# Optimization experiments

Hardware: AMD Instinct MI355X
Metric: run time of the kernel (lower is better)

Reference implementation:

```python
import jax, jax.numpy as jnp
import numpy as np

B, S, D = 4, 4096, 2048
SCAN, STATE = 128, 16


def setup_inputs() -> dict:
    key = jax.random.key(0)
    ks = jax.random.split(key, 8)
    scale = 1.0 / np.sqrt(D)
    scale_s = 1.0 / np.sqrt(SCAN)
    x = jax.random.normal(ks[0], (B, S, D), dtype=jnp.float32)
    Wi = jax.random.normal(ks[1], (SCAN, D), dtype=jnp.float32) * scale
    Wo = jax.random.normal(ks[2], (D, SCAN), dtype=jnp.float32) * 0.02  # torch zero-inits; small random for nontrivial output
    A_log = jax.random.normal(ks[3], (SCAN, STATE), dtype=jnp.float32) * 0.1
    Wb = jax.random.normal(ks[4], (STATE, SCAN), dtype=jnp.float32) * scale_s
    Wc = jax.random.normal(ks[5], (STATE, SCAN), dtype=jnp.float32) * scale_s
    Wdt = jax.random.normal(ks[6], (SCAN, SCAN), dtype=jnp.float32) * scale_s
    b_dt = jnp.full((SCAN,), -3.0, dtype=jnp.float32)
    Wg = jax.random.normal(ks[7], (SCAN, D), dtype=jnp.float32) * scale
    return {"x": x, "Wi": Wi, "Wo": Wo, "A_log": A_log, "Wb": Wb,
            "Wc": Wc, "Wdt": Wdt, "b_dt": b_dt, "Wg": Wg}


def _selective_scan_ffn(x, Wi, Wo, A_log, Wb, Wc, Wdt, b_dt, Wg):
    z = jnp.einsum('bsd,nd->bsn', x, Wi)                      # [B,S,SCAN]
    gate = jax.nn.silu(jnp.einsum('bsd,nd->bsn', x, Wg))      # [B,S,SCAN]
    A = -jnp.exp(A_log)                                        # [SCAN,STATE]
    B_in = jnp.einsum('bsn,kn->bsk', z, Wb)                   # [B,S,STATE]
    C_in = jnp.einsum('bsn,kn->bsk', z, Wc)                   # [B,S,STATE]
    dt = jax.nn.softplus(jnp.einsum('bsn,mn->bsm', z, Wdt) + b_dt)  # [B,S,SCAN]
    A_bar = 1.0 + dt[..., None] * A                            # [B,S,SCAN,STATE]

    def step(state, inp):
        a_t, dt_t, z_t, b_t, c_t = inp
        # state: [B,SCAN,STATE]
        state = a_t * state + dt_t[..., None] * (z_t[..., None] * b_t[:, None, :])
        y = jnp.einsum('bnk,bk->bn', state, c_t)               # [B,SCAN]
        return state, y

    xs = (jnp.moveaxis(A_bar, 1, 0), jnp.moveaxis(dt, 1, 0),
          jnp.moveaxis(z, 1, 0), jnp.moveaxis(B_in, 1, 0), jnp.moveaxis(C_in, 1, 0))
    state0 = jnp.zeros((x.shape[0], Wi.shape[0], A_log.shape[1]), dtype=x.dtype)
    _, ys = jax.lax.scan(step, state0, xs)                     # [S,B,SCAN]
    y = jnp.moveaxis(ys, 0, 1) * gate                          # [B,S,SCAN]
    return jnp.einsum('bsn,dn->bsd', y, Wo)                    # [B,S,D]


def reference(x, Wi, Wo, A_log, Wb, Wc, Wdt, b_dt, Wg):
    return _selective_scan_ffn(x, Wi, Wo, A_log, Wb, Wc, Wdt, b_dt, Wg)
```

## Files before the change

### kernel.cpp

```cpp
#include <hip/hip_runtime.h>
#include <hip/hip_bf16.h>
#include <math.h>

using bf16 = __hip_bfloat16;
typedef __attribute__((ext_vector_type(8))) short bf16x8;
typedef __attribute__((ext_vector_type(8))) short short8;
typedef __attribute__((ext_vector_type(4))) short short4v;
typedef __attribute__((ext_vector_type(4))) float f32x4;

#define AS1 __attribute__((address_space(1)))
#define AS3 __attribute__((address_space(3)))

constexpr int BATCH = 4;
constexpr int SEQ   = 4096;
constexpr int DIM   = 2048;
constexpr int SCAN  = 128;
constexpr int STATE = 16;
constexpr int LCH   = 16;
constexpr int NCH   = SEQ / LCH;

__device__ __forceinline__ float bf2f(bf16 v) { return __bfloat162float(v); }
__device__ __forceinline__ bf16  f2bf(float v) { return __float2bfloat16(v); }
__device__ __forceinline__ float bfbits(unsigned short u) {
  return __uint_as_float((unsigned)u << 16);
}

__device__ __forceinline__ int probe_dtype(const unsigned short* __restrict__ xp) {
  int cnt = 0;
  for (int i = 0; i < 512; ++i) {
    int e = (xp[i] >> 7) & 0xFF;
    cnt += (e >= 107 && e <= 147) ? 1 : 0;
  }
  return (cnt >= 410) ? 1 : 0;
}

__device__ __forceinline__ void conv_b(const void* src, bf16* dst, int n, int f,
                                       int gtid, int nt) {
  if (f) { const bf16* s = (const bf16*)src;  for (int i = gtid; i < n; i += nt) dst[i] = s[i]; }
  else   { const float* s = (const float*)src; for (int i = gtid; i < n; i += nt) dst[i] = f2bf(s[i]); }
}
__device__ __forceinline__ void conv_f(const void* src, float* dst, int n, int f,
                                       int gtid, int nt) {
  if (f) { const bf16* s = (const bf16*)src;  for (int i = gtid; i < n; i += nt) dst[i] = bf2f(s[i]); }
  else   { const float* s = (const float*)src; for (int i = gtid; i < n; i += nt) dst[i] = s[i]; }
}
__device__ __forceinline__ void conv_aneg(const void* src, float* dst, int n, int f,
                                          int gtid, int nt) {
  if (f) { const bf16* s = (const bf16*)src;  for (int i = gtid; i < n; i += nt) dst[i] = -expf(bf2f(s[i])); }
  else   { const float* s = (const float*)src; for (int i = gtid; i < n; i += nt) dst[i] = -expf(s[i]); }
}

__global__ __launch_bounds__(256) void kconv_w(
    const unsigned short* __restrict__ xprobe,
    const void* Wi, const void* Wg, const void* Wo, const void* Wdt,
    const void* Wb, const void* Wc, const void* bdt, const void* Alog,
    bf16* Wzg, bf16* Wob, bf16* Wdtb, bf16* Wbb, bf16* Wcb,
    float* bdtf, float* Anegf, int* __restrict__ flag) {
  int f = probe_dtype(xprobe);
  if (blockIdx.x == 0 && threadIdx.x == 0) *flag = f;
  int nt = gridDim.x * blockDim.x;
  int g  = blockIdx.x * blockDim.x + threadIdx.x;
  conv_b(Wi,  Wzg,               SCAN * DIM,  f, g, nt);
  conv_b(Wg,  Wzg + SCAN * DIM,  SCAN * DIM,  f, g, nt);
  conv_b(Wo,  Wob,  DIM * SCAN,  f, g, nt);
  conv_b(Wdt, Wdtb, SCAN * SCAN, f, g, nt);
  conv_b(Wb,  Wbb,  STATE * SCAN, f, g, nt);
  conv_b(Wc,  Wcb,  STATE * SCAN, f, g, nt);
  conv_f(bdt,  bdtf,  SCAN,          f, g, nt);
  conv_aneg(Alog, Anegf, SCAN * STATE, f, g, nt);
}

__device__ __forceinline__ int swzb(int row, int colbyte) {
  return row * 128 + (colbyte ^ ((row & 7) << 4));
}

struct ARegs { float4 v; };

template <int F>
__device__ __forceinline__ ARegs loadA(const void* __restrict__ xin, size_t rowbase,
                                       int k0, int ae) {
  ARegs r;
  if (F) {
    float2 t = *(const float2*)((const bf16*)xin + rowbase + k0 + ae);
    r.v.x = t.x; r.v.y = t.y; r.v.z = 0.f; r.v.w = 0.f;
  } else {
    r.v = *(const float4*)((const float*)xin + rowbase + k0 + ae);
  }
  return r;
}

template <int F>
__device__ __forceinline__ void writeA(char* abuf, int ar, int ae, const ARegs& rg) {
  char* d = abuf + swzb(ar, ae * 2);
  if (F) {
    *(float2*)d = make_float2(rg.v.x, rg.v.y);
  } else {
    union { float2 f2; bf16 b[4]; } u;
    u.b[0] = f2bf(rg.v.x); u.b[1] = f2bf(rg.v.y);
    u.b[2] = f2bf(rg.v.z); u.b[3] = f2bf(rg.v.w);
    *(float2*)d = u.f2;
  }
}

__device__ __forceinline__ void stageB(const bf16* __restrict__ W, int k0,
                                       char* bbuf, int tid) {
  int w = tid >> 6;
#pragma unroll
  for (int i = 0; i < 2; ++i) {
    int off = i * 16384 + tid * 16;
    int r   = off >> 7;
    int cbl = off & 127;
    int cbs = cbl ^ ((r & 7) << 4);
    const bf16* src = W + (size_t)r * DIM + k0 + (cbs >> 1);
    char* lb = bbuf + i * 16384 + w * 1024;
    __builtin_amdgcn_global_load_lds((const AS1 void*)src, (AS3 void*)lb, 16, 0, 0);
  }
}

__device__ __forceinline__ void compute64x256_16w(const char* abuf, const char* bbuf,
                                                  int tid, f32x4 acc[2][2]) {
  int l = tid & 63, w = tid >> 6;
  int wr = (w >> 3) * 32;
  int wc = (w & 7) * 32;
  int lr = l & 15, lk = (l >> 4) * 8;
#pragma unroll
  for (int kk = 0; kk < 64; kk += 32) {
    int cb = (kk + lk) * 2;
    bf16x8 a[2], b[2];
#pragma unroll
    for (int m = 0; m < 2; ++m)
      a[m] = *(const bf16x8*)(abuf + swzb(wr + m * 16 + lr, cb));
#pragma unroll
    for (int n = 0; n < 2; ++n)
      b[n] = *(const bf16x8*)(bbuf + swzb(wc + n * 16 + lr, cb));
#pragma unroll
    for (int m = 0; m < 2; ++m)
#pragma unroll
      for (int n = 0; n < 2; ++n)
        acc[m][n] = __builtin_amdgcn_mfma_f32_16x16x32_bf16(a[m], b[n], acc[m][n], 0, 0, 0);
  }
}

__device__ __forceinline__ void vm_wait3() { asm volatile("s_waitcnt vmcnt(3)" ::: "memory"); __builtin_amdgcn_sched_barrier(0); }
__device__ __forceinline__ void vm_wait0() { asm volatile("s_waitcnt vmcnt(0)" ::: "memory"); __builtin_amdgcn_sched_barrier(0); }
__device__ __forceinline__ void lgkm0_barrier() {
  asm volatile("s_waitcnt lgkmcnt(0)" ::: "memory");
  __builtin_amdgcn_sched_barrier(0);
  __builtin_amdgcn_s_barrier();
}

template <int F>
__device__ __forceinline__ void k1_main(const void* __restrict__ xin,
                                        const bf16* __restrict__ W,
                                        char* lds, size_t xrow, int ar, int ae,
                                        int tid, f32x4 acc[2][2]) {
  constexpr int NK = DIM / 64;
  constexpr int BUF = 40960;
  ARegs aH = loadA<F>(xin, xrow, 0, ae);
  stageB(W, 0, lds + 0 * BUF + 8192, tid);
  ARegs aN = loadA<F>(xin, xrow, 64, ae);
  stageB(W, 64, lds + 1 * BUF + 8192, tid);
  vm_wait3();
  writeA<F>(lds + 0 * BUF, ar, ae, aH);
  aH = aN;
  lgkm0_barrier();

  for (int t = 0; t < NK; ++t) {
    char* curb = lds + (t % 3) * BUF;
    if (t + 2 < NK) {
      aN = loadA<F>(xin, xrow, (t + 2) * 64, ae);
      stageB(W, (t + 2) * 64, lds + ((t + 2) % 3) * BUF + 8192, tid);
    }
    compute64x256_16w(curb, curb + 8192, tid, acc);
    if (t + 1 < NK) {
      if (t + 2 < NK) vm_wait3();
      else            vm_wait0();
      writeA<F>(lds + ((t + 1) % 3) * BUF, ar, ae, aH);
      aH = aN;
      lgkm0_barrier();
    }
  }
}

__global__ __launch_bounds__(1024) void k12_zg(const void* __restrict__ xin,
                                               const bf16* __restrict__ Wzg,
                                               const bf16* __restrict__ Wdtb,
                                               const bf16* __restrict__ Wbb,
                                               const bf16* __restrict__ Wcb,
                                               const float* __restrict__ bdtf,
                                               const float* __restrict__ Aneg,
                                               bf16* __restrict__ z,
                                               bf16* __restrict__ gate,
                                               float* __restrict__ dt,
                                               float* __restrict__ Bv,
                                               float* __restrict__ Cv,
                                               float* __restrict__ fin,
                                               float* __restrict__ apr,
                                               const int* __restrict__ flag) {
  __shared__ char lds[122880];
  int tid = threadIdx.x;
  int mb  = blockIdx.x;
  int m0  = mb * 64;
  int f   = *flag;
  int ar  = tid >> 4;
  int ae  = (tid & 15) * 4;
  size_t xrow = ((size_t)m0 + ar) * DIM;

  f32x4 acc[2][2];
#pragma unroll
  for (int m = 0; m < 2; ++m)
#pragma unroll
    for (int n = 0; n < 2; ++n)
#pragma unroll
      for (int j = 0; j < 4; ++j) acc[m][n][j] = 0.f;

  if (f) k1_main<1>(xin, Wzg, lds, xrow, ar, ae, tid, acc);
  else   k1_main<0>(xin, Wzg, lds, xrow, ar, ae, tid, acc);

  __syncthreads();

  bf16 (*zl)[128]   = (bf16 (*)[128])(lds);
  bf16 (*wl)[136]   = (bf16 (*)[136])(lds + 16384);
  bf16 (*dtlb)[128] = (bf16 (*)[128])(lds + 59904);
  bf16 (*Blcb)[16]  = (bf16 (*)[16]) (lds + 76288);

  {
    int l = tid & 63, w = tid >> 6;
    int wr = (w >> 3) * 32;
    int wcg = (w & 7) * 32;
    int sel = wcg >> 7;
    int cb  = wcg & 127;
    int lr = l & 15, lj = (l >> 4) * 4;
    bf16* o = sel ? gate : z;
#pragma unroll
    for (int m = 0; m < 2; ++m)
#pragma unroll
      for (int n = 0; n < 2; ++n)
#pragma unroll
        for (int j = 0; j < 4; ++j) {
          int rowl = wr + m * 16 + lj + j;
          int col  = cb + n * 16 + lr;
          float v = acc[m][n][j];
          if (sel) v = v / (1.f + expf(-v));
          bf16 bv = f2bf(v);
          o[(size_t)(m0 + rowl) * SCAN + col] = bv;
          if (!sel) zl[rowl][col] = bv;
        }
  }
  for (int idx = tid; idx < 160 * 16; idx += 1024) {
    int r = idx >> 4, c8 = (idx & 15) << 3;
    const bf16* src;
    if (r < 128)      src = Wdtb + r * 128;
    else if (r < 144) src = Wbb + (r - 128) * 128;
    else              src = Wcb + (r - 144) * 128;
    *(short8*)&wl[r][c8] = *(const short8*)(src + c8);
  }
  __syncthreads();

  if (tid < 256) {
    int l = tid & 63, w = tid >> 6;
    int lr = l & 15, lk = (l >> 4) * 8, lj = (l >> 4) * 4;
    f32x4 acc2[10];
#pragma unroll
    for (int n = 0; n < 10; ++n)
#pragma unroll
      for (int j = 0; j < 4; ++j) acc2[n][j] = 0.f;

#pragma unroll
    for (int kk = 0; kk < 128; kk += 32) {
      bf16x8 a = *(const bf16x8*)&zl[w * 16 + lr][kk + lk];
#pragma unroll
      for (int n = 0; n < 10; ++n) {
        bf16x8 bfr = *(const bf16x8*)&wl[n * 16 + lr][kk + lk];
        acc2[n] = __builtin_amdgcn_mfma_f32_16x16x32_bf16(a, bfr, acc2[n], 0, 0, 0);
      }
    }

#pragma unroll
    for (int n = 0; n < 10; ++n) {
      int o = n * 16 + lr;
#pragma unroll
      for (int j = 0; j < 4; ++j) {
        int row = w * 16 + lj + j;
        float v = acc2[n][j];
        if (o < 128) {
          v += bdtf[o];
          v = fmaxf(v, 0.f) + log1pf(expf(-fabsf(v)));
          dt[(size_t)(m0 + row) * SCAN + o] = v;
          dtlb[row][o] = f2bf(v);
        } else if (o < 144) {
          Bv[(size_t)(m0 + row) * STATE + (o - 128)] = v;
          Blcb[row][o - 128] = f2bf(v);
        } else {
          Cv[(size_t)(m0 + row) * STATE + (o - 144)] = v;
        }
      }
    }
  }
  __syncthreads();

  if (tid < 512) {
    int n  = tid & 127;
    int cc = tid >> 7;
    int b   = m0 >> 12;
    int ch0 = (m0 & 4095) >> 4;
    float A[STATE];
#pragma unroll
    for (int k = 0; k < STATE; ++k) A[k] = Aneg[n * STATE + k];

    float st[STATE], ap[STATE];
#pragma unroll
    for (int k = 0; k < STATE; ++k) { st[k] = 0.f; ap[k] = 1.f; }
#pragma unroll
    for (int t = 0; t < LCH; ++t) {
      int row = cc * LCH + t;
      float d = bf2f(dtlb[row][n]);
      float u = d * bf2f(zl[row][n]);
#pragma unroll
      for (int kg = 0; kg < 4; ++kg) {
        unsigned long long bb = *(const unsigned long long*)&Blcb[row][kg * 4];
        float b0 = bfbits((unsigned short)bb);
        float b1 = bfbits((unsigned short)(bb >> 16));
        float b2 = bfbits((unsigned short)(bb >> 32));
        float b3 = bfbits((unsigned short)(bb >> 48));
        float a;
        a = fmaf(d, A[kg*4+0], 1.f); st[kg*4+0] = fmaf(a, st[kg*4+0], u * b0); ap[kg*4+0] *= a;
        a = fmaf(d, A[kg*4+1], 1.f); st[kg*4+1] = fmaf(a, st[kg*4+1], u * b1); ap[kg*4+1] *= a;
        a = fmaf(d, A[kg*4+2], 1.f); st[kg*4+2] = fmaf(a, st[kg*4+2], u * b2); ap[kg*4+2] *= a;
        a = fmaf(d, A[kg*4+3], 1.f); st[kg*4+3] = fmaf(a, st[kg*4+3], u * b3); ap[kg*4+3] *= a;
      }
    }
    size_t base = ((size_t)b * NCH + (ch0 + cc)) * (STATE * SCAN) + n;
#pragma unroll
    for (int k = 0; k < STATE; ++k) {
      fin[base + k * SCAN] = st[k];
      apr[base + k * SCAN] = ap[k];
    }
  }
}

__global__ __launch_bounds__(64) void k3b(const float* __restrict__ fin,
                                          float* __restrict__ apr) {
  int c  = blockIdx.x * 64 + threadIdx.x;
  int b  = c >> 11;
  int kn = c & 2047;
  size_t base = (size_t)b * NCH * 2048 + kn;
  float s = 0.f;
  for (int g = 0; g < NCH; g += 16) {
    float fv[16], av[16];
#pragma unroll
    for (int i = 0; i < 16; ++i) {
      size_t o = base + (size_t)(g + i) * 2048;
      fv[i] = fin[o];
      av[i] = apr[o];
    }
#pragma unroll
    for (int i = 0; i < 16; ++i) {
      size_t o = base + (size_t)(g + i) * 2048;
      apr[o] = s;
      s = fmaf(av[i], s, fv[i]);
    }
  }
}

__global__ __launch_bounds__(128) void k3c(
    const float* __restrict__ dt, const bf16* z,
    const float* __restrict__ Bv, const float* __restrict__ Cv,
    const float* __restrict__ Aneg, const float* __restrict__ inc,
    const bf16* __restrict__ gate, bf16* yg) {
  __shared__ float Bl[LCH][STATE];
  __shared__ float Cl[LCH][STATE];
  int n  = threadIdx.x;
  int ch = blockIdx.x, b = blockIdx.y;
  int t0 = ch * LCH;
  if (n < LCH * STATE / 4)
    ((float4*)&Bl[0][0])[n] = ((const float4*)(Bv + ((size_t)b * SEQ + t0) * STATE))[n];
  else if (n < LCH * STATE / 2)
    ((float4*)&Cl[0][0])[n - LCH * STATE / 4] =
        ((const float4*)(Cv + ((size_t)b * SEQ + t0) * STATE))[n - LCH * STATE / 4];

  size_t base = ((size_t)b * NCH + ch) * (STATE * SCAN) + n;
  float A[STATE], st[STATE];
#pragma unroll
  for (int k = 0; k < STATE; ++k) {
    A[k]  = Aneg[n * STATE + k];
    st[k] = inc[base + k * SCAN];
  }
  __syncthreads();

  const float* dtp = dt   + ((size_t)b * SEQ + t0) * SCAN + n;
  const bf16*  zp  = z    + ((size_t)b * SEQ + t0) * SCAN + n;
  const bf16*  gp  = gate + ((size_t)b * SEQ + t0) * SCAN + n;
  bf16*        yp  = yg   + ((size_t)b * SEQ + t0) * SCAN + n;
#pragma unroll 4
  for (int t = 0; t < LCH; ++t) {
    float d = dtp[t * SCAN];
    float u = d * bf2f(zp[t * SCAN]);
    float g = bf2f(gp[t * SCAN]);
    float y0 = 0.f, y1 = 0.f, y2 = 0.f, y3 = 0.f;
#pragma unroll
    for (int kg = 0; kg < 4; ++kg) {
      float4 B4 = *(const float4*)&Bl[t][kg * 4];
      float4 C4 = *(const float4*)&Cl[t][kg * 4];
      float a, p = 0.f;
      a = fmaf(d, A[kg*4+0], 1.f); st[kg*4+0] = fmaf(a, st[kg*4+0], u * B4.x); p = fmaf(st[kg*4+0], C4.x, p);
      a = fmaf(d, A[kg*4+1], 1.f); st[kg*4+1] = fmaf(a, st[kg*4+1], u * B4.y); p = fmaf(st[kg*4+1], C4.y, p);
      a = fmaf(d, A[kg*4+2], 1.f); st[kg*4+2] = fmaf(a, st[kg*4+2], u * B4.z); p = fmaf(st[kg*4+2], C4.z, p);
      a = fmaf(d, A[kg*4+3], 1.f); st[kg*4+3] = fmaf(a, st[kg*4+3], u * B4.w); p = fmaf(st[kg*4+3], C4.w, p);
      if (kg == 0) y0 = p; else if (kg == 1) y1 = p; else if (kg == 2) y2 = p; else y3 = p;
    }
    float y = (y0 + y1) + (y2 + y3);
    yp[t * SCAN] = f2bf(y * g);
  }
}

__device__ __forceinline__ int swz256(int row, int colbyte) {
  return row * 256 + (colbyte ^ ((row & 7) << 4));
}

__global__ __launch_bounds__(256) void k4_out(const bf16* __restrict__ yg,
                                              const bf16* __restrict__ Wo,
                                              void* __restrict__ outv,
                                              const int* __restrict__ flag) {
  __shared__ char lds[49152];
  int tid = threadIdx.x;
  int mb = blockIdx.x, nb = blockIdx.y;
  int w = tid >> 6;

#pragma unroll
  for (int i = 0; i < 8; ++i) {
    int off = i * 4096 + tid * 16;
    int r   = off >> 8;
    int cbl = off & 255;
    int cbs = cbl ^ ((r & 7) << 4);
    const bf16* src = yg + (size_t)(mb * 128 + r) * SCAN + (cbs >> 1);
    __builtin_amdgcn_global_load_lds((const AS1 void*)src,
                                     (AS3 void*)(lds + i * 4096 + w * 1024), 16, 0, 0);
  }
#pragma unroll
  for (int i = 0; i < 4; ++i) {
    int off = i * 4096 + tid * 16;
    int r   = off >> 8;
    int cbl = off & 255;
    int cbs = cbl ^ ((r & 7) << 4);
    const bf16* src = Wo + (size_t)(nb * 64 + r) * SCAN + (cbs >> 1);
    __builtin_amdgcn_global_load_lds((const AS1 void*)src,
                                     (AS3 void*)(lds + 32768 + i * 4096 + w * 1024), 16, 0, 0);
  }
  __syncthreads();

  int l = tid & 63;
  int lr = l & 15, lk = (l >> 4) * 8;
  f32x4 acc[2][4];
#pragma unroll
  for (int m = 0; m < 2; ++m)
#pragma unroll
    for (int n = 0; n < 4; ++n)
#pragma unroll
      for (int j = 0; j < 4; ++j) acc[m][n][j] = 0.f;

#pragma unroll
  for (int kk = 0; kk < 128; kk += 32) {
    int cb = (kk + lk) * 2;
    bf16x8 a[2], b[4];
#pragma unroll
    for (int m = 0; m < 2; ++m)
      a[m] = *(const bf16x8*)(lds + swz256(w * 32 + m * 16 + lr, cb));
#pragma unroll
    for (int n = 0; n < 4; ++n)
      b[n] = *(const bf16x8*)(lds + 32768 + swz256(n * 16 + lr, cb));
#pragma unroll
    for (int m = 0; m < 2; ++m)
#pragma unroll
      for (int n = 0; n < 4; ++n)
        acc[m][n] = __builtin_amdgcn_mfma_f32_16x16x32_bf16(a[m], b[n], acc[m][n], 0, 0, 0);
  }

  int f = *flag;
  int lj = (l >> 4) * 4;
#pragma unroll
  for (int m = 0; m < 2; ++m)
#pragma unroll
    for (int n = 0; n < 4; ++n)
#pragma unroll
      for (int j = 0; j < 4; ++j) {
        int row = mb * 128 + w * 32 + m * 16 + lj + j;
        int col = nb * 64 + n * 16 + lr;
        size_t off = (size_t)row * DIM + col;
        float v = acc[m][n][j];
        if (f) ((bf16*)outv)[off] = f2bf(v);
        else   ((float*)outv)[off] = v;
      }
}

extern "C" void kernel_launch(void* const* d_in, const int* in_sizes, int n_in,
                              void* d_out, int out_size, void* d_ws, size_t ws_size,
                              hipStream_t stream) {
  const void* x     = d_in[0];
  const void* Wi    = d_in[1];
  const void* Wo    = d_in[2];
  const void* A_log = d_in[3];
  const void* Wb    = d_in[4];
  const void* Wc    = d_in[5];
  const void* Wdt   = d_in[6];
  const void* b_dt  = d_in[7];
  const void* Wg    = d_in[8];

  const size_t M = (size_t)BATCH * SEQ;
  char* p = (char*)d_ws;
  int*   flag = (int*)p;    p += 256;
  bf16*  Wzg  = (bf16*)p;   p += (size_t)2 * SCAN * DIM * 2;
  bf16*  Wob  = (bf16*)p;   p += (size_t)DIM * SCAN * 2;
  bf16*  Wdtb = (bf16*)p;   p += (size_t)SCAN * SCAN * 2;
  bf16*  Wbb  = (bf16*)p;   p += (size_t)STATE * SCAN * 2;
  bf16*  Wcb  = (bf16*)p;   p += (size_t)STATE * SCAN * 2;
  float* bdtf = (float*)p;  p += SCAN * 4;
  float* Anegf= (float*)p;  p += (size_t)SCAN * STATE * 4;
  bf16*  z    = (bf16*)p;   p += M * SCAN * 2;
  bf16*  gate = (bf16*)p;   p += M * SCAN * 2;
  bf16*  yg   = z;
  float* dt   = (float*)p;  p += M * SCAN * 4;
  float* Bv   = (float*)p;  p += M * STATE * 4;
  float* Cv   = (float*)p;  p += M * STATE * 4;
  float* fin  = (float*)p;  p += (size_t)BATCH * NCH * SCAN * STATE * 4;
  float* apr  = (float*)p;  p += (size_t)BATCH * NCH * SCAN * STATE * 4;

  kconv_w <<<256, 256, 0, stream>>>((const unsigned short*)x,
                                    Wi, Wg, Wo, Wdt, Wb, Wc, b_dt, A_log,
                                    Wzg, Wob, Wdtb, Wbb, Wcb, bdtf, Anegf, flag);
  k12_zg  <<<dim3(256), 1024, 0, stream>>>(x, Wzg, Wdtb, Wbb, Wcb, bdtf, Anegf,
                                           z, gate, dt, Bv, Cv, fin, apr, flag);
  k3b     <<<dim3(128), 64, 0, stream>>>(fin, apr);
  k3c     <<<dim3(NCH, BATCH), 128, 0, stream>>>(dt, z, Bv, Cv, Anegf, apr, gate, yg);
  k4_out  <<<dim3(128, 32), 256, 0, stream>>>(yg, Wob, d_out, flag);
}
```

Baseline: 139.9 us.

## Widen K-tile to 128 and switch to double-buffered LDS pipeline in zg GEMM

The fused z/gate projection GEMM now processes K in steps of 128 instead of 64, with wider per-thread A loads (8 elements) and a 256-byte swizzled LDS row layout. The triple-buffered prefetch-two-ahead pipeline is replaced by a double buffer with one-ahead prefetch and a full vmcnt(0) wait, which halves the number of barriers per K sweep. LDS use grows to 160 KB, and the pipeline has less prefetch slack, so global-load latency may be exposed.

```diff
diff --git a/kernel.cpp b/kernel.cpp
--- a/kernel.cpp
+++ b/kernel.cpp
@@ -5,7 +5,6 @@
 using bf16 = __hip_bfloat16;
 typedef __attribute__((ext_vector_type(8))) short bf16x8;
 typedef __attribute__((ext_vector_type(8))) short short8;
-typedef __attribute__((ext_vector_type(4))) short short4v;
 typedef __attribute__((ext_vector_type(4))) float f32x4;
 
 #define AS1 __attribute__((address_space(1)))
@@ -23,6 +22,10 @@
 __device__ __forceinline__ bf16  f2bf(float v) { return __float2bfloat16(v); }
 __device__ __forceinline__ float bfbits(unsigned short u) {
   return __uint_as_float((unsigned)u << 16);
+}
+
+__device__ __forceinline__ int swz256(int row, int colbyte) {
+  return row * 256 + (colbyte ^ ((row & 7) << 4));
 }
 
 __device__ __forceinline__ int probe_dtype(const unsigned short* __restrict__ xp) {
@@ -70,35 +73,32 @@
   conv_aneg(Alog, Anegf, SCAN * STATE, f, g, nt);
 }
 
-__device__ __forceinline__ int swzb(int row, int colbyte) {
-  return row * 128 + (colbyte ^ ((row & 7) << 4));
-}
-
-struct ARegs { float4 v; };
+struct ARegs { float4 v[2]; };
 
 template <int F>
 __device__ __forceinline__ ARegs loadA(const void* __restrict__ xin, size_t rowbase,
                                        int k0, int ae) {
   ARegs r;
   if (F) {
-    float2 t = *(const float2*)((const bf16*)xin + rowbase + k0 + ae);
-    r.v.x = t.x; r.v.y = t.y; r.v.z = 0.f; r.v.w = 0.f;
+    r.v[0] = *(const float4*)((const bf16*)xin + rowbase + k0 + ae);
   } else {
-    r.v = *(const float4*)((const float*)xin + rowbase + k0 + ae);
+    const float4* s = (const float4*)((const float*)xin + rowbase + k0 + ae);
+    r.v[0] = s[0]; r.v[1] = s[1];
   }
   return r;
 }
 
 template <int F>
 __device__ __forceinline__ void writeA(char* abuf, int ar, int ae, const ARegs& rg) {
-  char* d = abuf + swzb(ar, ae * 2);
+  char* d = abuf + swz256(ar, ae * 2);
   if (F) {
-    *(float2*)d = make_float2(rg.v.x, rg.v.y);
+    *(float4*)d = rg.v[0];
   } else {
-    union { float2 f2; bf16 b[4]; } u;
-    u.b[0] = f2bf(rg.v.x); u.b[1] = f2bf(rg.v.y);
-    u.b[2] = f2bf(rg.v.z); u.b[3] = f2bf(rg.v.w);
-    *(float2*)d = u.f2;
+    union { short8 s; bf16 b[8]; } u;
+    const float* fv = (const float*)&rg.v[0];
+#pragma unroll
+    for (int i = 0; i < 8; ++i) u.b[i] = f2bf(fv[i]);
+    *(short8*)d = u.s;
   }
 }
 
@@ -106,10 +106,10 @@
                                        char* bbuf, int tid) {
   int w = tid >> 6;
 #pragma unroll
-  for (int i = 0; i < 2; ++i) {
+  for (int i = 0; i < 4; ++i) {
     int off = i * 16384 + tid * 16;
-    int r   = off >> 7;
-    int cbl = off & 127;
+    int r   = off >> 8;
+    int cbl = off & 255;
     int cbs = cbl ^ ((r & 7) << 4);
     const bf16* src = W + (size_t)r * DIM + k0 + (cbs >> 1);
     char* lb = bbuf + i * 16384 + w * 1024;
@@ -117,22 +117,22 @@
   }
 }
 
-__device__ __forceinline__ void compute64x256_16w(const char* abuf, const char* bbuf,
-                                                  int tid, f32x4 acc[2][2]) {
+__device__ __forceinline__ void compute64x256_k128(const char* abuf, const char* bbuf,
+                                                   int tid, f32x4 acc[2][2]) {
   int l = tid & 63, w = tid >> 6;
   int wr = (w >> 3) * 32;
   int wc = (w & 7) * 32;
   int lr = l & 15, lk = (l >> 4) * 8;
 #pragma unroll
-  for (int kk = 0; kk < 64; kk += 32) {
+  for (int kk = 0; kk < 128; kk += 32) {
     int cb = (kk + lk) * 2;
     bf16x8 a[2], b[2];
 #pragma unroll
     for (int m = 0; m < 2; ++m)
-      a[m] = *(const bf16x8*)(abuf + swzb(wr + m * 16 + lr, cb));
+      a[m] = *(const bf16x8*)(abuf + swz256(wr + m * 16 + lr, cb));
 #pragma unroll
     for (int n = 0; n < 2; ++n)
-      b[n] = *(const bf16x8*)(bbuf + swzb(wc + n * 16 + lr, cb));
+      b[n] = *(const bf16x8*)(bbuf + swz256(wc + n * 16 + lr, cb));
 #pragma unroll
     for (int m = 0; m < 2; ++m)
 #pragma unroll
@@ -141,7 +141,6 @@
   }
 }
 
-__device__ __forceinline__ void vm_wait3() { asm volatile("s_waitcnt vmcnt(3)" ::: "memory"); __builtin_amdgcn_sched_barrier(0); }
 __device__ __forceinline__ void vm_wait0() { asm volatile("s_waitcnt vmcnt(0)" ::: "memory"); __builtin_amdgcn_sched_barrier(0); }
 __device__ __forceinline__ void lgkm0_barrier() {
   asm volatile("s_waitcnt lgkmcnt(0)" ::: "memory");
@@ -154,29 +153,27 @@
                                         const bf16* __restrict__ W,
                                         char* lds, size_t xrow, int ar, int ae,
                                         int tid, f32x4 acc[2][2]) {
-  constexpr int NK = DIM / 64;
-  constexpr int BUF = 40960;
-  ARegs aH = loadA<F>(xin, xrow, 0, ae);
-  stageB(W, 0, lds + 0 * BUF + 8192, tid);
-  ARegs aN = loadA<F>(xin, xrow, 64, ae);
-  stageB(W, 64, lds + 1 * BUF + 8192, tid);
-  vm_wait3();
-  writeA<F>(lds + 0 * BUF, ar, ae, aH);
-  aH = aN;
-  lgkm0_barrier();
-
+  constexpr int NK  = DIM / 128;
+  constexpr int BUF = 81920;
+  {
+    ARegs a0 = loadA<F>(xin, xrow, 0, ae);
+    stageB(W, 0, lds + 16384, tid);
+    vm_wait0();
+    writeA<F>(lds, ar, ae, a0);
+    lgkm0_barrier();
+  }
   for (int t = 0; t < NK; ++t) {
-    char* curb = lds + (t % 3) * BUF;
-    if (t + 2 < NK) {
-      aN = loadA<F>(xin, xrow, (t + 2) * 64, ae);
-      stageB(W, (t + 2) * 64, lds + ((t + 2) % 3) * BUF + 8192, tid);
-    }
-    compute64x256_16w(curb, curb + 8192, tid, acc);
+    char* cur = lds + (t & 1) * BUF;
+    char* nxt = lds + ((t + 1) & 1) * BUF;
+    ARegs aN;
     if (t + 1 < NK) {
-      if (t + 2 < NK) vm_wait3();
-      else            vm_wait0();
-      writeA<F>(lds + ((t + 1) % 3) * BUF, ar, ae, aH);
-      aH = aN;
+      aN = loadA<F>(xin, xrow, (t + 1) * 128, ae);
+      stageB(W, (t + 1) * 128, nxt + 16384, tid);
+    }
+    compute64x256_k128(cur, cur + 16384, tid, acc);
+    if (t + 1 < NK) {
+      vm_wait0();
+      writeA<F>(nxt, ar, ae, aN);
       lgkm0_barrier();
     }
   }
@@ -197,13 +194,13 @@
                                                float* __restrict__ fin,
                                                float* __restrict__ apr,
                                                const int* __restrict__ flag) {
-  __shared__ char lds[122880];
+  __shared__ char lds[163840];
   int tid = threadIdx.x;
   int mb  = blockIdx.x;
   int m0  = mb * 64;
   int f   = *flag;
   int ar  = tid >> 4;
-  int ae  = (tid & 15) * 4;
+  int ae  = (tid & 15) * 8;
   size_t xrow = ((size_t)m0 + ar) * DIM;
 
   f32x4 acc[2][2];
@@ -412,10 +409,6 @@
     float y = (y0 + y1) + (y2 + y3);
     yp[t * SCAN] = f2bf(y * g);
   }
-}
-
-__device__ __forceinline__ int swz256(int row, int colbyte) {
-  return row * 256 + (colbyte ^ ((row & 7) << 4));
 }
 
 __global__ __launch_bounds__(256) void k4_out(const bf16* __restrict__ yg,
```

Result: no change. 142.1 us (+1.6%).
